# Kernel tuning notes

Hardware: AMD Instinct MI355X
Metric: run time of the kernel (lower is better)

The kernel has to match this reference:

```python
import math
import jax, jax.numpy as jnp
import numpy as np

B, T, DIM = 2, 2048, 2048
HEADS, HEAD_DIM = 16, 128
KV_GROUPS = 4
N_KV = HEADS // KV_GROUPS  # 4
LATENT = 512
SEL_TOPK, SEL_HEADS, SEL_DIM = 64, 1, 64
SOFTCAP = 30.0
EPS = 1e-6


def _alibi_slopes(n):
    def pot(p):
        start = 2.0 ** (-(2.0 ** (-(math.log2(p) - 3))))
        return [start * start ** i for i in range(p)]
    if math.log2(n).is_integer():
        return pot(n)
    cp = 2 ** int(math.floor(math.log2(n)))
    s = pot(cp)
    s += _alibi_slopes(2 * cp)[0::2][: n - cp]
    return s


def _alibi_bias(h, t):
    slopes = jnp.asarray(_alibi_slopes(h), jnp.float32)
    pos = jnp.arange(t)
    dist = jnp.clip(pos[:, None] - pos[None, :], 0, None).astype(jnp.float32)  # causal clamp_min(0)
    return -slopes[:, None, None] * dist  # (H,T,T)


def _rope_emb(t, d):
    inv = 1.0 / (10000.0 ** (jnp.arange(0, d, 2, dtype=jnp.float32) / d))
    f = jnp.arange(t, dtype=jnp.float32)[:, None] * inv[None, :]
    return jnp.concatenate([f, f], axis=-1)  # (T, D)


def _apply_rotary(x, emb):
    # x: (B,T,H,D); replicates RotaryPositionalEncoding.apply_rotary exactly
    cos = jnp.cos(emb)[None, :, None, :]
    sin = jnp.sin(emb)[None, :, None, :]
    x1, x2 = x[..., 0::2], x[..., 1::2]
    c, s = cos[..., 0::2], sin[..., 0::2]
    r = jnp.stack([x1 * c - x2 * s, x1 * s + x2 * c], axis=-1)
    return r.reshape(x.shape)


def _rmsnorm(x, w):
    return x * jax.lax.rsqrt(jnp.mean(x * x, axis=-1, keepdims=True) + EPS) * w


def _forward(x, w_q, b_q, w_down, b_down, w_up, b_up, w_o, b_o, qn_w, kn_w, gate_w, gate_b):
    b, t, _ = x.shape
    # MLA projections
    q = (x @ w_q + b_q).reshape(b, t, HEADS, HEAD_DIM)
    kv = (x @ w_down + b_down) @ w_up + b_up  # (B,T,2*N_KV*D)
    k = kv[..., : N_KV * HEAD_DIM].reshape(b, t, N_KV, HEAD_DIM)
    v = kv[..., N_KV * HEAD_DIM:].reshape(b, t, N_KV, HEAD_DIM)
    # QK RMS-norm + RoPE
    q = _rmsnorm(q, qn_w)
    k = _rmsnorm(k, kn_w)
    emb = _rope_emb(t, HEAD_DIM)
    q = _apply_rotary(q, emb)
    k = _apply_rotary(k, emb)
    # GQA expand kv heads
    k = jnp.repeat(k, KV_GROUPS, axis=2)
    v = jnp.repeat(v, KV_GROUPS, axis=2)
    q = q.transpose(0, 2, 1, 3)  # (B,H,T,D)
    k = k.transpose(0, 2, 1, 3)
    v = v.transpose(0, 2, 1, 3)
    # selector top-k mask (detached)
    qs = jax.lax.stop_gradient(q[:, :SEL_HEADS, :, :SEL_DIM].astype(jnp.float32))
    ks = jax.lax.stop_gradient(k[:, :SEL_HEADS, :, :SEL_DIM].astype(jnp.float32))
    s = jnp.einsum('bhqd,bhkd->bhqk', qs, ks) / math.sqrt(SEL_DIM)
    tri = jnp.triu(jnp.ones((t, t), bool), 1)  # future positions
    s = jnp.where(tri, -jnp.inf, s)
    idx = jax.lax.top_k(s, SEL_TOPK)[1]  # (B,hs,T,K)
    sel = jnp.zeros((b, SEL_HEADS, t, t), bool)
    bi = jnp.arange(b)[:, None, None, None]
    hi = jnp.arange(SEL_HEADS)[None, :, None, None]
    ti = jnp.arange(t)[None, None, :, None]
    sel = sel.at[bi, hi, ti, idx].set(True)
    sel = sel | jnp.eye(t, dtype=bool)[None, None]  # always keep diagonal
    sel = sel & ~tri  # causal
    sel = jnp.any(sel, axis=1, keepdims=True)  # broadcast over heads (h_sel < h)
    amask = jnp.where(sel, 0.0, -jnp.inf).astype(jnp.float32)
    # attention with softcap + ALiBi
    scores = jnp.einsum('bhqd,bhkd->bhqk', q, k) / math.sqrt(HEAD_DIM)
    scores = jnp.tanh(scores / SOFTCAP) * SOFTCAP
    scores = scores + _alibi_bias(HEADS, t)[None] + amask
    attn = jax.nn.softmax(scores, axis=-1)
    y = jnp.einsum('bhqk,bhkd->bhqd', attn, v)
    # per-head dense sigmoid gating on output
    gate = jax.nn.sigmoid(jnp.einsum('bhtd,hde->bhte', y, gate_w) + gate_b[None, :, None, :])
    y = (y * gate).transpose(0, 2, 1, 3).reshape(b, t, HEADS * HEAD_DIM)
    return y @ w_o + b_o


def setup_inputs() -> dict:
    key = jax.random.key(0)
    ks = jax.random.split(key, 6)
    sd = 0.02
    return {
        'x': jax.random.normal(ks[0], (B, T, DIM), jnp.float32),
        'w_q': jax.random.normal(ks[1], (DIM, HEADS * HEAD_DIM), jnp.float32) * sd,
        'b_q': jnp.zeros((HEADS * HEAD_DIM,), jnp.float32),
        'w_down': jax.random.normal(ks[2], (DIM, LATENT), jnp.float32) * sd,
        'b_down': jnp.zeros((LATENT,), jnp.float32),
        'w_up': jax.random.normal(ks[3], (LATENT, 2 * N_KV * HEAD_DIM), jnp.float32) * sd,
        'b_up': jnp.zeros((2 * N_KV * HEAD_DIM,), jnp.float32),
        'w_o': jax.random.normal(ks[4], (HEADS * HEAD_DIM, DIM), jnp.float32) * sd,
        'b_o': jnp.zeros((DIM,), jnp.float32),
        'qn_w': jnp.ones((HEAD_DIM,), jnp.float32),
        'kn_w': jnp.ones((HEAD_DIM,), jnp.float32),
        'gate_w': jax.random.normal(ks[5], (HEADS, HEAD_DIM, HEAD_DIM), jnp.float32) * (1.0 / math.sqrt(HEAD_DIM)),
        'gate_b': jnp.zeros((HEADS, HEAD_DIM), jnp.float32),
    }


def reference(x, w_q, b_q, w_down, b_down, w_up, b_up, w_o, b_o, qn_w, kn_w, gate_w, gate_b):
    return _forward(x, w_q, b_q, w_down, b_down, w_up, b_up, w_o, b_o, qn_w, kn_w, gate_w, gate_b)
```

## Files before the change

kernel.cpp:

```cpp
#include <hip/hip_runtime.h>
#include <math.h>

#define T_SEQ 2048
#define BATCH 2
#define NHEADS 16
#define HD 128
#define NKV 4

typedef __bf16 bf16x8 __attribute__((ext_vector_type(8)));
typedef float f32x4 __attribute__((ext_vector_type(4)));

__device__ inline unsigned short bf16rne(float f) {
  unsigned u = __float_as_uint(f);
  unsigned r = (u + 0x7FFFu + ((u >> 16) & 1u)) >> 16;
  return (unsigned short)r;
}

__device__ inline float bflo(unsigned u) {
  return __uint_as_float(u << 16);
}
__device__ inline float bfhi(unsigned u) {
  return __uint_as_float(u & 0xFFFF0000u);
}

__device__ inline void gload_lds16(const void* g, void* l) {
  __builtin_amdgcn_global_load_lds(
      (__attribute__((address_space(1))) void*)const_cast<void*>(g),
      (__attribute__((address_space(3))) void*)l, 16, 0, 0);
}

#define ENC_NEGINF 0x007FFFFFu
__device__ inline unsigned enc32(float v) {
  unsigned u = __float_as_uint(v);
  return (u & 0x80000000u) ? ~u : (u | 0x80000000u);
}

__global__ void rope_table_kernel(float* __restrict__ tab) {
  int t = blockIdx.x;
  int i = threadIdx.x;
  int j = (2 * i) & 63;
  float y = (float)pow(10000.0, (double)j / 64.0);
  float invf = 1.0f / y;
  float angle = (float)t * invf;
  double a = (double)angle;
  tab[(t * 64 + i) * 2 + 0] = (float)cos(a);
  tab[(t * 64 + i) * 2 + 1] = (float)sin(a);
}

__global__ __launch_bounds__(128) void norm_rope_kernel(
    float* __restrict__ base, const float* __restrict__ w,
    const float* __restrict__ tab, int Hloc, int rowStride) {
  int blk = blockIdx.x;
  int h = blk % Hloc;
  int bt = blk / Hloc;
  int t = bt & (T_SEQ - 1);
  float* row = base + (size_t)bt * rowStride + h * HD;
  int d = threadIdx.x;
  float v = row[d];
  __shared__ float red[128];
  red[d] = v * v;
  __syncthreads();
#pragma unroll
  for (int off = 64; off > 0; off >>= 1) {
    if (d < off) red[d] += red[d + off];
    __syncthreads();
  }
  float ssum = red[0];
  __syncthreads();
  float inv = 1.0f / sqrtf(ssum / 128.0f + 1e-6f);
  float xn = v * inv * w[d];
  red[d] = xn;
  __syncthreads();
  int p = d >> 1;
  float c  = tab[(t * 64 + p) * 2 + 0];
  float sn = tab[(t * 64 + p) * 2 + 1];
  float x1 = red[p * 2], x2 = red[p * 2 + 1];
  row[d] = ((d & 1) == 0) ? (x1 * c - x2 * sn) : (x1 * sn + x2 * c);
}

#define BKG 16
__global__ __launch_bounds__(256) void sgemm3_kernel(
    const float* __restrict__ A,
    const float* __restrict__ W1, const float* __restrict__ bias1,
    float* __restrict__ C1, int ldw1, int ldc1, int nx1,
    const float* __restrict__ W2, const float* __restrict__ bias2,
    float* __restrict__ C2, int ldw2, int ldc2, int K) {
  __shared__ float As[BKG][68];
  __shared__ float Bs[BKG][68];
  int bx = blockIdx.x;
  const float* W; const float* bias; float* C; int ldw, ldc, n0;
  if (bx < nx1) {
    W = W1; bias = bias1; C = C1; ldw = ldw1; ldc = ldc1; n0 = bx * 64;
  } else {
    W = W2; bias = bias2; C = C2; ldw = ldw2; ldc = ldc2;
    n0 = (bx - nx1) * 64;
  }
  int tid = threadIdx.x;
  int tx = tid & 15;
  int ty = tid >> 4;
  int m0 = blockIdx.y * 64;
  int ar = tid >> 2, ac = (tid & 3) * 4;
  int brr = tid >> 4, bc = (tid & 15) * 4;
  const float* Ap = A + (size_t)(m0 + ar) * K + ac;
  const float* Wp = W + (size_t)brr * ldw + n0 + bc;
  float acc[4][4] = {};
  float4 av = *(const float4*)(Ap);
  float4 wv = *(const float4*)(Wp);
  for (int k0 = 0; k0 < K; k0 += BKG) {
    As[ac + 0][ar] = av.x; As[ac + 1][ar] = av.y;
    As[ac + 2][ar] = av.z; As[ac + 3][ar] = av.w;
    *(float4*)&Bs[brr][bc] = wv;
    __syncthreads();
    if (k0 + BKG < K) {
      av = *(const float4*)(Ap + k0 + BKG);
      wv = *(const float4*)(Wp + (size_t)(k0 + BKG) * ldw);
    }
#pragma unroll
    for (int kk = 0; kk < BKG; kk++) {
      float4 a = *(const float4*)&As[kk][ty * 4];
      float4 b = *(const float4*)&Bs[kk][tx * 4];
      float aa[4] = {a.x, a.y, a.z, a.w};
      float bb[4] = {b.x, b.y, b.z, b.w};
#pragma unroll
      for (int i = 0; i < 4; i++)
#pragma unroll
        for (int j = 0; j < 4; j++) acc[i][j] += aa[i] * bb[j];
    }
    __syncthreads();
  }
  float4 bv = *(const float4*)&bias[n0 + tx * 4];
  float bb[4] = {bv.x, bv.y, bv.z, bv.w};
#pragma unroll
  for (int i = 0; i < 4; i++) {
    float4 o;
    o.x = acc[i][0] + bb[0];
    o.y = acc[i][1] + bb[1];
    o.z = acc[i][2] + bb[2];
    o.w = acc[i][3] + bb[3];
    *(float4*)&C[(size_t)(m0 + ty * 4 + i) * ldc + n0 + tx * 4] = o;
  }
}

__global__ __launch_bounds__(256) void mfma_gemm_bt(
    const unsigned short* __restrict__ A,
    const unsigned short* __restrict__ BT,
    const float* __restrict__ bias,
    float* __restrict__ C,
    int M, int N, int K) {
  __shared__ bf16x8 lA[16][64];
  __shared__ bf16x8 lB[16][64];
  int tid = threadIdx.x;
  int w = tid >> 6, lane = tid & 63;
  int m0 = blockIdx.y * 128, n0 = blockIdx.x * 128;
  int wm = w >> 1, wn = w & 1;
  f32x4 acc[4][4] = {};
  int sr = lane & 15;
  int sk = (lane >> 4) * 8;
  const unsigned short* Abase = A + (size_t)(m0 + sr) * K + sk;
  const unsigned short* Bbase = BT + (size_t)(n0 + sr) * K + sk;

  for (int k0 = 0; k0 < K; k0 += 64) {
    __syncthreads();
#pragma unroll
    for (int c = 0; c < 4; c++) {
      int ch = w * 4 + c;
      int tt = ch >> 1, kk = ch & 1;
      gload_lds16(Abase + (size_t)(tt * 16) * K + k0 + kk * 32, &lA[ch][0]);
      gload_lds16(Bbase + (size_t)(tt * 16) * K + k0 + kk * 32, &lB[ch][0]);
    }
    __syncthreads();
#pragma unroll
    for (int kk = 0; kk < 2; kk++) {
      bf16x8 af[4], bfr[4];
#pragma unroll
      for (int t = 0; t < 4; t++) {
        af[t]  = lA[(wm * 4 + t) * 2 + kk][lane];
        bfr[t] = lB[(wn * 4 + t) * 2 + kk][lane];
      }
#pragma unroll
      for (int i = 0; i < 4; i++)
#pragma unroll
        for (int j = 0; j < 4; j++)
          acc[i][j] = __builtin_amdgcn_mfma_f32_16x16x32_bf16(
              af[i], bfr[j], acc[i][j], 0, 0, 0);
    }
  }
  int col0 = n0 + wn * 64 + (lane & 15);
  int row0 = m0 + wm * 64 + (lane >> 4) * 4;
#pragma unroll
  for (int j = 0; j < 4; j++) {
    float bv = bias[col0 + j * 16];
#pragma unroll
    for (int i = 0; i < 4; i++) {
#pragma unroll
      for (int r = 0; r < 4; r++)
        C[(size_t)(row0 + i * 16 + r) * N + col0 + j * 16] = acc[i][j][r] + bv;
    }
  }
}

__global__ __launch_bounds__(256) void convert_bf16_kernel(
    const float* __restrict__ X, unsigned short* __restrict__ Y, int n4) {
  int i = blockIdx.x * 256 + threadIdx.x;
  if (i >= n4) return;
  float4 v = ((const float4*)X)[i];
  ushort4 o;
  o.x = bf16rne(v.x); o.y = bf16rne(v.y);
  o.z = bf16rne(v.z); o.w = bf16rne(v.w);
  ((ushort4*)Y)[i] = o;
}

__global__ __launch_bounds__(256) void transpose_bf16_kernel(
    const float* __restrict__ W, unsigned short* __restrict__ WT,
    int K, int N) {
  __shared__ unsigned short t[32][33];
  int k0 = blockIdx.y * 32, n0 = blockIdx.x * 32;
  int tid = threadIdx.x;
#pragma unroll
  for (int i = 0; i < 4; i++) {
    int idx = tid + i * 256;
    int r = idx >> 5, c = idx & 31;
    t[c][r] = bf16rne(W[(size_t)(k0 + r) * N + n0 + c]);
  }
  __syncthreads();
#pragma unroll
  for (int i = 0; i < 4; i++) {
    int idx = tid + i * 256;
    int r = idx >> 5, c = idx & 31;
    WT[(size_t)(n0 + r) * K + k0 + c] = t[r][c];
  }
}

__global__ __launch_bounds__(256) void score_kernel(
    const float* __restrict__ qsel,
    const float* __restrict__ kv,
    unsigned* __restrict__ S,
    int b) {
  int tc = blockIdx.x, tr = blockIdx.y;
  if (tc > tr || tr == 0) return;
  __shared__ float qsT[64][68];
  __shared__ float ksT[64][68];
  int tid = threadIdx.x;
  int r0 = tr * 64, c0 = tc * 64;
#pragma unroll
  for (int u = 0; u < 16; u++) {
    int idx = u * 256 + tid;
    int row = idx >> 6, d = idx & 63;
    qsT[d][row] = qsel[((size_t)(b * T_SEQ + r0 + row)) * 128 + d];
  }
#pragma unroll
  for (int u = 0; u < 16; u++) {
    int idx = u * 256 + tid;
    int c = idx >> 6, d = idx & 63;
    ksT[d][c] = kv[((size_t)(b * T_SEQ + c0 + c)) * 1024 + d];
  }
  __syncthreads();
  int tx = tid & 15, ty = tid >> 4;
  float acc[4][4] = {};
  for (int d = 0; d < 64; d++) {
    float4 qv = *(const float4*)&qsT[d][ty * 4];
    float4 kx = *(const float4*)&ksT[d][tx * 4];
    float qq[4] = {qv.x, qv.y, qv.z, qv.w};
    float kk[4] = {kx.x, kx.y, kx.z, kx.w};
#pragma unroll
    for (int i = 0; i < 4; i++)
#pragma unroll
      for (int j = 0; j < 4; j++) acc[i][j] += qq[i] * kk[j];
  }
#pragma unroll
  for (int i = 0; i < 4; i++) {
    int r = r0 + ty * 4 + i;
    uint4 o;
    int c = c0 + tx * 4;
    o.x = (c + 0 <= r) ? enc32(acc[i][0] * 0.125f) : ENC_NEGINF;
    o.y = (c + 1 <= r) ? enc32(acc[i][1] * 0.125f) : ENC_NEGINF;
    o.z = (c + 2 <= r) ? enc32(acc[i][2] * 0.125f) : ENC_NEGINF;
    o.w = (c + 3 <= r) ? enc32(acc[i][3] * 0.125f) : ENC_NEGINF;
    *(uint4*)&S[(size_t)r * 2048 + c] = o;
  }
}

__global__ __launch_bounds__(256) void select_topk_kernel(
    const unsigned* __restrict__ S,
    int* __restrict__ sel_cnt, int* __restrict__ sel_idx, int b) {
  int blk = blockIdx.x;
  int r0 = blk * 4;
  int tid = threadIdx.x;

  if (r0 < 64) {
    for (int j = 0; j < 4; j++) {
      int r = r0 + j;
      int row = b * T_SEQ + r;
      if (tid == 0) sel_cnt[row] = r + 1;
      for (int c = tid; c <= r; c += 256) sel_idx[row * 66 + c] = c;
    }
    return;
  }

  int wv = tid >> 6, lane = tid & 63;
  int rr = r0 + wv;
  int row = b * T_SEQ + rr;
  int imax = rr >> 6;

  unsigned e[32];
  const unsigned* Sp = S + (size_t)rr * 2048 + lane;
#pragma unroll
  for (int i = 0; i < 32; i++) e[i] = (i <= imax) ? Sp[i * 64] : ENC_NEGINF;

  unsigned t = 0;
  for (int bit = 31; bit >= 0; --bit) {
    unsigned cand = t | (1u << bit);
    int cnt = 0;
#pragma unroll
    for (int i = 0; i < 32; i++) cnt += (e[i] >= cand) ? 1 : 0;
#pragma unroll
    for (int off = 1; off < 64; off <<= 1) cnt += __shfl_xor(cnt, off);
    if (cnt >= 64) t = cand;
  }

  unsigned long long below = (lane == 63) ? 0x7FFFFFFFFFFFFFFFull
                                          : ((1ull << lane) - 1ull);
  bool hasdiag = false;
  int base = 0;
#pragma unroll
  for (int i = 0; i < 32; i++) {
    int c = i * 64 + lane;
    bool wn = (e[i] > t);
    unsigned long long m = __ballot(wn);
    if (wn) {
      int slot = base + (int)__popcll(m & below);
      sel_idx[(size_t)row * 66 + slot] = c;
      if (c == rr) hasdiag = true;
    }
    base += (int)__popcll(m);
  }
  int g = base;
  int need = 64 - g;
  int tb = 0;
#pragma unroll
  for (int i = 0; i < 32; i++) {
    int c = i * 64 + lane;
    bool tie = (e[i] == t);
    unsigned long long m = __ballot(tie);
    int rank = tb + (int)__popcll(m & below);
    if (tie && rank < need) {
      sel_idx[(size_t)row * 66 + g + rank] = c;
      if (c == rr) hasdiag = true;
    }
    tb += (int)__popcll(m);
  }
  unsigned long long hd = __ballot(hasdiag);
  if (lane == 0) {
    sel_cnt[row] = hd ? 64 : 65;
    if (!hd) sel_idx[(size_t)row * 66 + 64] = rr;
  }
}

__global__ __launch_bounds__(256) void attn_kernel(
    const float* __restrict__ q,
    const unsigned short* __restrict__ kvb,
    const int* __restrict__ sel_cnt, const int* __restrict__ sel_idx,
    float* __restrict__ yg) {
  int blk = blockIdx.x;
  int g = blk & 3;
  int br = blk >> 2;
  int b = br >> 11;
  int r = br & (T_SEQ - 1);
  int tid = threadIdx.x;
  int lane = tid & 63, wv = tid >> 6;
  int H = g * 4 + wv;

  __shared__ unsigned kls[65 * 64];
  __shared__ float pbuf[4][68];
  __shared__ int idxs[66];

  int cnt = sel_cnt[br];
  if (tid < 66) idxs[tid] = (tid < cnt) ? sel_idx[(size_t)br * 66 + tid] : 0;
  __syncthreads();

  for (int c = tid; c < 65 * 16; c += 256) {
    int row = c >> 4, part = c & 15;
    uint4 kd = make_uint4(0u, 0u, 0u, 0u);
    if (row < cnt) {
      const unsigned short* gp = kvb
          + ((size_t)(b * T_SEQ + idxs[row])) * 1024 + g * HD + part * 8;
      kd = *(const uint4*)gp;
    }
    int slot = part ^ (row & 15);
    *(uint4*)&kls[row * 64 + slot * 4] = kd;
  }
  __syncthreads();

  double sd = 1.0;
  for (int i = 0; i <= H; i++) sd *= 0.70710678118654752440;
  float slope = (float)sd;

  const float* qrow = q + (size_t)br * 2048 + H * HD;

  int kidx = idxs[min(lane, cnt - 1)];
  int swz = lane & 15;
  const unsigned* kr = &kls[lane * 64];
  float acc = 0.f;
#pragma unroll
  for (int dd = 0; dd < 16; dd++) {
    uint4 kb = *(const uint4*)&kr[(dd ^ swz) * 4];
    float4 qa = *(const float4*)(qrow + dd * 8);
    float4 qb = *(const float4*)(qrow + dd * 8 + 4);
    acc += qa.x * bflo(kb.x) + qa.y * bfhi(kb.x);
    acc += qa.z * bflo(kb.y) + qa.w * bfhi(kb.y);
    acc += qb.x * bflo(kb.z) + qb.y * bfhi(kb.z);
    acc += qb.z * bflo(kb.w) + qb.w * bfhi(kb.w);
  }
  float sca = acc / sqrtf(128.0f);
  float tch = tanhf(sca / 30.0f) * 30.0f;
  float s = (lane < cnt) ? (tch - slope * (float)(r - kidx)) : -INFINITY;

  float stail = -INFINITY;
  if (cnt == 65) {
    int i64 = idxs[64];
    unsigned u = kls[64 * 64 + lane];
    float2 qt = *(const float2*)(qrow + 2 * lane);
    float ta = qt.x * bflo(u) + qt.y * bfhi(u);
#pragma unroll
    for (int off = 32; off > 0; off >>= 1) ta += __shfl_xor(ta, off);
    stail = tanhf(ta / sqrtf(128.0f) / 30.0f) * 30.0f
            - slope * (float)(r - i64);
  }

  float m = s;
#pragma unroll
  for (int off = 32; off > 0; off >>= 1) m = fmaxf(m, __shfl_xor(m, off));
  m = fmaxf(m, stail);
  float e = (lane < cnt) ? expf(s - m) : 0.f;
  float sum = e;
#pragma unroll
  for (int off = 32; off > 0; off >>= 1) sum += __shfl_xor(sum, off);
  float et = (cnt == 65) ? expf(stail - m) : 0.f;
  sum += et;
  pbuf[wv][lane] = e / sum;
  if (lane == 0) pbuf[wv][64] = et / sum;
  if (lane >= 1 && lane <= 3) pbuf[wv][64 + lane] = 0.f;

  const unsigned short* vbase = kvb + (size_t)b * T_SEQ * 1024 + 512 + g * HD;
  float y0 = 0.f, y1 = 0.f;
  int jmax = (cnt + 3) >> 2;
  for (int j4 = 0; j4 < jmax; j4++) {
    float4 p4 = *(const float4*)&pbuf[wv][j4 * 4];
    float pp[4] = {p4.x, p4.y, p4.z, p4.w};
#pragma unroll
    for (int t = 0; t < 4; t++) {
      int ij = idxs[min(j4 * 4 + t, cnt - 1)];
      unsigned u = *(const unsigned*)(vbase + (size_t)ij * 1024 + 2 * lane);
      y0 += pp[t] * bflo(u);
      y1 += pp[t] * bfhi(u);
    }
  }
  float2 o;
  o.x = y0;
  o.y = y1;
  *(float2*)(yg + (size_t)br * 2048 + H * HD + 2 * lane) = o;
}

__global__ __launch_bounds__(256) void gate_kernel(
    float* __restrict__ yg, const float* __restrict__ gw,
    const float* __restrict__ gb) {
  int blk = blockIdx.x;
  int h = blk & 15;
  int bt0 = (blk >> 4) * 16;
  int tid = threadIdx.x;
  __shared__ float ys[16][128];
  for (int i = tid; i < 16 * 128; i += 256) {
    int rr = i >> 7, d = i & 127;
    ys[rr][d] = yg[(size_t)(bt0 + rr) * 2048 + h * HD + d];
  }
  __syncthreads();
  int e = tid & 127;
  int rblk = tid >> 7;
  const float* gwp = gw + (size_t)h * 16384 + e;
  float acc[8] = {};
  for (int d = 0; d < 128; d++) {
    float wval = gwp[(size_t)d * 128];
#pragma unroll
    for (int k = 0; k < 8; k++) acc[k] += ys[rblk * 8 + k][d] * wval;
  }
  float bb = gb[h * 128 + e];
#pragma unroll
  for (int k = 0; k < 8; k++) {
    int rr = rblk * 8 + k;
    float gate = 1.f / (1.f + expf(-(acc[k] + bb)));
    yg[(size_t)(bt0 + rr) * 2048 + h * HD + e] = ys[rr][e] * gate;
  }
}

extern "C" void kernel_launch(void* const* d_in, const int* in_sizes, int n_in,
                              void* d_out, int out_size, void* d_ws, size_t ws_size,
                              hipStream_t stream) {
  const float* x      = (const float*)d_in[0];
  const float* w_q    = (const float*)d_in[1];
  const float* b_q    = (const float*)d_in[2];
  const float* w_down = (const float*)d_in[3];
  const float* b_down = (const float*)d_in[4];
  const float* w_up   = (const float*)d_in[5];
  const float* b_up   = (const float*)d_in[6];
  const float* w_o    = (const float*)d_in[7];
  const float* b_o    = (const float*)d_in[8];
  const float* qn_w   = (const float*)d_in[9];
  const float* kn_w   = (const float*)d_in[10];
  const float* gate_w = (const float*)d_in[11];
  const float* gate_b = (const float*)d_in[12];

  float* ws    = (float*)d_ws;
  float* kvbuf = ws;
  float* yg    = ws + 4194304;
  float* dlat  = yg;
  float* tab   = ws + 12582912;
  int*   cnt   = (int*)(ws + 12845056);
  int*   sidx  = cnt + 4096;
  float* qsel  = ws + 13120000;
  unsigned short* xb  = (unsigned short*)(ws + 13906432);
  unsigned short* dlatb = xb;
  unsigned short* ygb = xb;
  unsigned* Sbuf = (unsigned*)xb;
  unsigned short* wT  = xb + 8388608;
  unsigned short* wupT = wT;
  unsigned short* kvb  = wT;

  float* qbuf = (float*)d_out;
  const int BT = BATCH * T_SEQ;

  rope_table_kernel<<<T_SEQ, 64, 0, stream>>>(tab);
  convert_bf16_kernel<<<8192, 256, 0, stream>>>(x, xb, 2097152);
  transpose_bf16_kernel<<<dim3(64, 64), 256, 0, stream>>>(w_q, wT, 2048, 2048);
  mfma_gemm_bt<<<dim3(16, 32), 256, 0, stream>>>(xb, wT, b_q, qbuf,
                                                 BT, 2048, 2048);
  sgemm3_kernel<<<dim3(10, 64), 256, 0, stream>>>(
      x, w_q, b_q, qsel, 2048, 128, 2,
      w_down, b_down, dlat, 512, 512, 2048);
  convert_bf16_kernel<<<2048, 256, 0, stream>>>(dlat, dlatb, 524288);
  transpose_bf16_kernel<<<dim3(32, 16), 256, 0, stream>>>(w_up, wupT,
                                                          512, 1024);
  mfma_gemm_bt<<<dim3(8, 32), 256, 0, stream>>>(dlatb, wupT, b_up, kvbuf,
                                                BT, 1024, 512);
  sgemm3_kernel<<<dim3(2, 64), 256, 0, stream>>>(
      dlat, w_up, b_up, kvbuf, 1024, 1024, 2,
      w_up, b_up, kvbuf, 1024, 1024, 512);
  norm_rope_kernel<<<BT * 16, 128, 0, stream>>>(qbuf, qn_w, tab, 16, 2048);
  norm_rope_kernel<<<BT, 128, 0, stream>>>(qsel, qn_w, tab, 1, 128);
  norm_rope_kernel<<<BT * 4, 128, 0, stream>>>(kvbuf, kn_w, tab, 4, 1024);
  convert_bf16_kernel<<<4096, 256, 0, stream>>>(kvbuf, kvb, 1048576);
  for (int b = 0; b < BATCH; b++) {
    score_kernel<<<dim3(32, 32), 256, 0, stream>>>(qsel, kvbuf, Sbuf, b);
    select_topk_kernel<<<512, 256, 0, stream>>>(Sbuf, cnt, sidx, b);
  }
  attn_kernel<<<BT * 4, 256, 0, stream>>>(qbuf, kvb, cnt, sidx, yg);
  gate_kernel<<<(BT / 16) * 16, 256, 0, stream>>>(yg, gate_w, gate_b);
  convert_bf16_kernel<<<8192, 256, 0, stream>>>(yg, ygb, 2097152);
  transpose_bf16_kernel<<<dim3(64, 64), 256, 0, stream>>>(w_o, wT, 2048, 2048);
  mfma_gemm_bt<<<dim3(16, 32), 256, 0, stream>>>(ygb, wT, b_o, (float*)d_out,
                                                 BT, 2048, 2048);
}
```

Measured before the change: 773.7 us.

## Fuse bf16 conversions into norm/gate kernels, warp-shuffle q norm, deeper sgemm k-tile

Fuses the K/V bf16 conversion into a dedicated kv RMS-norm+RoPE kernel and the gated output's bf16 conversion into the gate kernel, removing two separate conversion passes over global memory. Replaces the block-reduction q norm with a wave-per-row kernel using shuffles and float2 accesses. Doubles the fp32 sgemm k-tile to 32 to halve barrier count, at the cost of more shared memory and registers.

```diff
diff --git a/kernel.cpp b/kernel.cpp
--- a/kernel.cpp
+++ b/kernel.cpp
@@ -78,15 +78,74 @@
   row[d] = ((d & 1) == 0) ? (x1 * c - x2 * sn) : (x1 * sn + x2 * c);
 }
 
-#define BKG 16
-__global__ __launch_bounds__(256) void sgemm3_kernel(
+__global__ __launch_bounds__(128) void kvnorm_rope_kernel(
+    float* __restrict__ base, const float* __restrict__ w,
+    const float* __restrict__ tab, unsigned short* __restrict__ kvb) {
+  int blk = blockIdx.x;
+  int h = blk % 4;
+  int bt = blk / 4;
+  int t = bt & (T_SEQ - 1);
+  float* row = base + (size_t)bt * 1024 + h * HD;
+  int d = threadIdx.x;
+  float v = row[d];
+  __shared__ float red[128];
+  red[d] = v * v;
+  __syncthreads();
+#pragma unroll
+  for (int off = 64; off > 0; off >>= 1) {
+    if (d < off) red[d] += red[d + off];
+    __syncthreads();
+  }
+  float ssum = red[0];
+  __syncthreads();
+  float inv = 1.0f / sqrtf(ssum / 128.0f + 1e-6f);
+  float xn = v * inv * w[d];
+  red[d] = xn;
+  __syncthreads();
+  int p = d >> 1;
+  float c  = tab[(t * 64 + p) * 2 + 0];
+  float sn = tab[(t * 64 + p) * 2 + 1];
+  float x1 = red[p * 2], x2 = red[p * 2 + 1];
+  float out = ((d & 1) == 0) ? (x1 * c - x2 * sn) : (x1 * sn + x2 * c);
+  row[d] = out;
+  size_t kb = (size_t)bt * 1024 + h * HD + d;
+  kvb[kb] = bf16rne(out);
+  float vv = base[(size_t)bt * 1024 + 512 + h * HD + d];
+  kvb[(size_t)bt * 1024 + 512 + h * HD + d] = bf16rne(vv);
+}
+
+__global__ __launch_bounds__(256) void qnorm_rope_kernel(
+    float* __restrict__ base, const float* __restrict__ w,
+    const float* __restrict__ tab) {
+  int row = blockIdx.x * 4 + (threadIdx.x >> 6);
+  int lane = threadIdx.x & 63;
+  int h = row & 15;
+  int bt = row >> 4;
+  int t = bt & (T_SEQ - 1);
+  float* rp = base + (size_t)bt * 2048 + h * HD;
+  float2 v = *(const float2*)(rp + 2 * lane);
+  float ss = v.x * v.x + v.y * v.y;
+#pragma unroll
+  for (int off = 32; off > 0; off >>= 1) ss += __shfl_xor(ss, off);
+  float inv = 1.0f / sqrtf(ss / 128.0f + 1e-6f);
+  float2 wv = *(const float2*)(w + 2 * lane);
+  float x1 = v.x * inv * wv.x;
+  float x2 = v.y * inv * wv.y;
+  float2 cs = *(const float2*)(tab + (t * 64 + lane) * 2);
+  float2 o;
+  o.x = x1 * cs.x - x2 * cs.y;
+  o.y = x1 * cs.y + x2 * cs.x;
+  *(float2*)(rp + 2 * lane) = o;
+}
+
+__global__ __launch_bounds__(256) void sgemm4_kernel(
     const float* __restrict__ A,
     const float* __restrict__ W1, const float* __restrict__ bias1,
     float* __restrict__ C1, int ldw1, int ldc1, int nx1,
     const float* __restrict__ W2, const float* __restrict__ bias2,
     float* __restrict__ C2, int ldw2, int ldc2, int K) {
-  __shared__ float As[BKG][68];
-  __shared__ float Bs[BKG][68];
+  __shared__ float As[32][68];
+  __shared__ float Bs[32][68];
   int bx = blockIdx.x;
   const float* W; const float* bias; float* C; int ldw, ldc, n0;
   if (bx < nx1) {
@@ -99,24 +158,31 @@
   int tx = tid & 15;
   int ty = tid >> 4;
   int m0 = blockIdx.y * 64;
-  int ar = tid >> 2, ac = (tid & 3) * 4;
-  int brr = tid >> 4, bc = (tid & 15) * 4;
+  int ar = tid >> 2, ac = (tid & 3) * 8;
+  int brr = tid >> 3, bc = (tid & 7) * 8;
   const float* Ap = A + (size_t)(m0 + ar) * K + ac;
   const float* Wp = W + (size_t)brr * ldw + n0 + bc;
   float acc[4][4] = {};
-  float4 av = *(const float4*)(Ap);
-  float4 wv = *(const float4*)(Wp);
-  for (int k0 = 0; k0 < K; k0 += BKG) {
-    As[ac + 0][ar] = av.x; As[ac + 1][ar] = av.y;
-    As[ac + 2][ar] = av.z; As[ac + 3][ar] = av.w;
-    *(float4*)&Bs[brr][bc] = wv;
+  float4 av0 = *(const float4*)(Ap);
+  float4 av1 = *(const float4*)(Ap + 4);
+  float4 wv0 = *(const float4*)(Wp);
+  float4 wv1 = *(const float4*)(Wp + 4);
+  for (int k0 = 0; k0 < K; k0 += 32) {
+    As[ac + 0][ar] = av0.x; As[ac + 1][ar] = av0.y;
+    As[ac + 2][ar] = av0.z; As[ac + 3][ar] = av0.w;
+    As[ac + 4][ar] = av1.x; As[ac + 5][ar] = av1.y;
+    As[ac + 6][ar] = av1.z; As[ac + 7][ar] = av1.w;
+    *(float4*)&Bs[brr][bc] = wv0;
+    *(float4*)&Bs[brr][bc + 4] = wv1;
     __syncthreads();
-    if (k0 + BKG < K) {
-      av = *(const float4*)(Ap + k0 + BKG);
-      wv = *(const float4*)(Wp + (size_t)(k0 + BKG) * ldw);
-    }
-#pragma unroll
-    for (int kk = 0; kk < BKG; kk++) {
+    if (k0 + 32 < K) {
+      av0 = *(const float4*)(Ap + k0 + 32);
+      av1 = *(const float4*)(Ap + k0 + 36);
+      wv0 = *(const float4*)(Wp + (size_t)(k0 + 32) * ldw);
+      wv1 = *(const float4*)(Wp + (size_t)(k0 + 32) * ldw + 4);
+    }
+#pragma unroll
+    for (int kk = 0; kk < 32; kk++) {
       float4 a = *(const float4*)&As[kk][ty * 4];
       float4 b = *(const float4*)&Bs[kk][tx * 4];
       float aa[4] = {a.x, a.y, a.z, a.w};
@@ -462,8 +528,8 @@
 }
 
 __global__ __launch_bounds__(256) void gate_kernel(
-    float* __restrict__ yg, const float* __restrict__ gw,
-    const float* __restrict__ gb) {
+    const float* __restrict__ yg, unsigned short* __restrict__ ygb,
+    const float* __restrict__ gw, const float* __restrict__ gb) {
   int blk = blockIdx.x;
   int h = blk & 15;
   int bt0 = (blk >> 4) * 16;
@@ -488,7 +554,7 @@
   for (int k = 0; k < 8; k++) {
     int rr = rblk * 8 + k;
     float gate = 1.f / (1.f + expf(-(acc[k] + bb)));
-    yg[(size_t)(bt0 + rr) * 2048 + h * HD + e] = ys[rr][e] * gate;
+    ygb[(size_t)(bt0 + rr) * 2048 + h * HD + e] = bf16rne(ys[rr][e] * gate);
   }
 }
 
@@ -533,7 +599,7 @@
   transpose_bf16_kernel<<<dim3(64, 64), 256, 0, stream>>>(w_q, wT, 2048, 2048);
   mfma_gemm_bt<<<dim3(16, 32), 256, 0, stream>>>(xb, wT, b_q, qbuf,
                                                  BT, 2048, 2048);
-  sgemm3_kernel<<<dim3(10, 64), 256, 0, stream>>>(
+  sgemm4_kernel<<<dim3(10, 64), 256, 0, stream>>>(
       x, w_q, b_q, qsel, 2048, 128, 2,
       w_down, b_down, dlat, 512, 512, 2048);
   convert_bf16_kernel<<<2048, 256, 0, stream>>>(dlat, dlatb, 524288);
@@ -541,20 +607,18 @@
                                                           512, 1024);
   mfma_gemm_bt<<<dim3(8, 32), 256, 0, stream>>>(dlatb, wupT, b_up, kvbuf,
                                                 BT, 1024, 512);
-  sgemm3_kernel<<<dim3(2, 64), 256, 0, stream>>>(
+  sgemm4_kernel<<<dim3(2, 64), 256, 0, stream>>>(
       dlat, w_up, b_up, kvbuf, 1024, 1024, 2,
       w_up, b_up, kvbuf, 1024, 1024, 512);
-  norm_rope_kernel<<<BT * 16, 128, 0, stream>>>(qbuf, qn_w, tab, 16, 2048);
+  qnorm_rope_kernel<<<BT * 4, 256, 0, stream>>>(qbuf, qn_w, tab);
   norm_rope_kernel<<<BT, 128, 0, stream>>>(qsel, qn_w, tab, 1, 128);
-  norm_rope_kernel<<<BT * 4, 128, 0, stream>>>(kvbuf, kn_w, tab, 4, 1024);
-  convert_bf16_kernel<<<4096, 256, 0, stream>>>(kvbuf, kvb, 1048576);
+  kvnorm_rope_kernel<<<BT * 4, 128, 0, stream>>>(kvbuf, kn_w, tab, kvb);
   for (int b = 0; b < BATCH; b++) {
     score_kernel<<<dim3(32, 32), 256, 0, stream>>>(qsel, kvbuf, Sbuf, b);
     select_topk_kernel<<<512, 256, 0, stream>>>(Sbuf, cnt, sidx, b);
   }
   attn_kernel<<<BT * 4, 256, 0, stream>>>(qbuf, kvb, cnt, sidx, yg);
-  gate_kernel<<<(BT / 16) * 16, 256, 0, stream>>>(yg, gate_w, gate_b);
-  convert_bf16_kernel<<<8192, 256, 0, stream>>>(yg, ygb, 2097152);
+  gate_kernel<<<(BT / 16) * 16, 256, 0, stream>>>(yg, ygb, gate_w, gate_b);
   transpose_bf16_kernel<<<dim3(64, 64), 256, 0, stream>>>(w_o, wT, 2048, 2048);
   mfma_gemm_bt<<<dim3(16, 32), 256, 0, stream>>>(ygb, wT, b_o, (float*)d_out,
                                                  BT, 2048, 2048);
```

After: 747.9 us. 3.3% less time.
